# Kernel optimization log

Measured on AMD Instinct MI355X. Metric: run time of the kernel, lower is better.

## Reference

```python
import math
import jax, jax.numpy as jnp
from jax import lax
import numpy as np

NEG_INF = -1e9
LOG_2PI = math.log(2.0 * math.pi)


def compute_logp(z_p, m_p, logs_p):
    # z_p: [B,C,Ty], m_p/logs_p: [B,C,Tx] -> logp: [B,Tx,Ty]
    o_scale = jnp.exp(-2.0 * logs_p)                                  # [B,C,Tx]
    logp1 = jnp.sum(-0.5 * LOG_2PI - logs_p, axis=1)[:, :, None]      # [B,Tx,1]
    logp2 = jnp.einsum('bct,bcs->bts', o_scale, -0.5 * z_p ** 2)      # [B,Tx,Ty]
    logp3 = jnp.einsum('bct,bcs->bts', m_p * o_scale, z_p)            # [B,Tx,Ty]
    logp4 = jnp.sum(-0.5 * m_p ** 2 * o_scale, axis=1)[:, :, None]    # [B,Tx,1]
    return logp1 + logp2 + logp3 + logp4


def maximum_path(logp, mask):
    # Monotonic alignment search (Glow-TTS/VITS Viterbi DP).
    # logp, mask: [B,Tx,Ty]. Returns hard alignment path [B,Tx,Ty] in {0,1}.
    B, Tx, Ty = logp.shape
    tx = mask[:, :, 0].sum(axis=1).astype(jnp.int32)   # text lengths [B]
    ty = mask[:, 0, :].sum(axis=1).astype(jnp.int32)   # mel lengths  [B]
    xs = jnp.arange(Tx, dtype=jnp.int32)

    # ---- forward DP over mel frames y ----
    def fwd(v, inp):
        y, col = inp                                   # col: logp[:, :, y]  [B,Tx]
        v_stay = jnp.where(xs[None, :] == y, NEG_INF, v)           # can't stay on diagonal
        first = jnp.where(y == 0, 0.0, NEG_INF)                     # x==0 boundary
        v_move = jnp.concatenate([jnp.broadcast_to(first, (B, 1)).astype(v.dtype), v[:, :-1]], axis=1)
        newv = jnp.maximum(v_stay, v_move) + col
        # feasible band: x <= y and enough frames remain to consume all text
        feas = (xs[None, :] <= y) & (xs[None, :] >= tx[:, None] + y - ty[:, None])
        newv = jnp.where(feas, newv, NEG_INF)
        return newv, newv

    cols = jnp.moveaxis(logp, 2, 0)                    # [Ty,B,Tx]
    init = jnp.full((B, Tx), NEG_INF, dtype=logp.dtype)
    _, vals = lax.scan(fwd, init, (jnp.arange(Ty, dtype=jnp.int32), cols))  # [Ty,B,Tx]
    prev = jnp.concatenate([jnp.zeros((1, B, Tx), dtype=vals.dtype), vals[:-1]], axis=0)

    # ---- backtrack from (tx-1, ty-1) down to y=0 ----
    def bwd(idx, inp):
        y, pv = inp                                    # pv: value column at y-1  [B,Tx]
        active = y < ty                                # [B] bool
        path_col = (active[:, None] & (xs[None, :] == idx[:, None])).astype(logp.dtype)
        v_stay = jnp.take_along_axis(pv, idx[:, None], axis=1)[:, 0]
        v_move = jnp.take_along_axis(pv, jnp.maximum(idx - 1, 0)[:, None], axis=1)[:, 0]
        dec = (idx != 0) & ((idx == y) | (v_stay < v_move))
        idx = jnp.where(active & dec, idx - 1, idx)
        return idx, path_col

    _, path = lax.scan(bwd, tx - 1, (jnp.arange(Ty, dtype=jnp.int32), prev), reverse=True)
    return jnp.transpose(path, (1, 2, 0))              # [B,Tx,Ty]


def setup_inputs() -> dict:
    key = jax.random.key(0)
    ks = jax.random.split(key, 5)
    B, C, Tx, Ty = 16, 192, 384, 1536
    z_p = jax.random.normal(ks[0], (B, C, Ty), dtype=jnp.float32)
    m_p = jax.random.normal(ks[1], (B, C, Tx), dtype=jnp.float32)
    logs_p = 0.5 * jax.random.normal(ks[2], (B, C, Tx), dtype=jnp.float32)
    x_len = jax.random.randint(ks[3], (B,), Tx // 2, Tx + 1)
    y_len = jax.random.randint(ks[4], (B,), Ty // 2, Ty + 1)  # Ty//2 > Tx -> path always feasible
    x_mask = (jnp.arange(Tx)[None, :] < x_len[:, None]).astype(jnp.float32)[:, None, :]
    y_mask = (jnp.arange(Ty)[None, :] < y_len[:, None]).astype(jnp.float32)[:, None, :]
    return {"z_p": z_p, "m_p": m_p, "logs_p": logs_p, "x_mask": x_mask, "y_mask": y_mask}


def reference(z_p, m_p, logs_p, x_mask, y_mask):
    # forward_mas_without_dp: log-likelihood einsum + monotonic alignment search
    attn_mask = x_mask[:, 0, :, None] * y_mask[:, 0, None, :]   # [B,Tx,Ty]
    logp = compute_logp(z_p, m_p, logs_p)
    attn = maximum_path(logp, attn_mask)
    return attn[:, None]                                         # [B,1,Tx,Ty]
```

## Files before the change

### kernel.cpp

```cpp
#include <hip/hip_runtime.h>
#include <hip/hip_bf16.h>
#include <math.h>

#define NEG_INF (-1e9f)
#define B_   16
#define C_   192
#define TX   384
#define TY   1536
#define NWP  49
#define ROW_BYTES 1536

#define BM 64
#define BN 64
#define BK 16

typedef float f32x2 __attribute__((ext_vector_type(2)));
typedef float f32x4 __attribute__((ext_vector_type(4)));

__global__ __launch_bounds__(64) void k_len(const float* __restrict__ xm,
                                            const float* __restrict__ ym,
                                            int* __restrict__ lens) {
    const int b = blockIdx.x, l = threadIdx.x;
    int tx = 0, ty = 0;
#pragma unroll
    for (int i = 0; i < TX / 64; ++i)
        tx += __popcll(__ballot(xm[b * TX + i * 64 + l] > 0.5f));
#pragma unroll
    for (int i = 0; i < TY / 64; ++i)
        ty += __popcll(__ballot(ym[b * TY + i * 64 + l] > 0.5f));
    if (l == 0) { lens[2 * b] = tx; lens[2 * b + 1] = ty; }
}

__global__ __launch_bounds__(128) void k_rowconst(const float* __restrict__ m_p,
                                                  const float* __restrict__ logs_p,
                                                  float* __restrict__ r) {
    const int b = blockIdx.y;
    const int t = blockIdx.x * 128 + threadIdx.x;
    const float* mp = m_p + b * C_ * TX + t;
    const float* lp = logs_p + b * C_ * TX + t;
    const float c0 = -0.9189385332046727f;
    float s = 0.0f;
    for (int c = 0; c < C_; ++c) {
        float ls = lp[c * TX];
        float m  = mp[c * TX];
        float os = expf(-2.0f * ls);
        s += (c0 - ls) - 0.5f * m * m * os;
    }
    r[b * TX + t] = s;
}

__global__ __launch_bounds__(256) void k_logp(const float* __restrict__ z_p,
                                              const float* __restrict__ m_p,
                                              const float* __restrict__ logs_p,
                                              const float* __restrict__ r,
                                              const int* __restrict__ lens,
                                              float* __restrict__ outT) {
    const int b   = blockIdx.z;
    const int sm0 = blockIdx.y * BM;
    const int ty_len = lens[2 * b + 1];
    if (sm0 >= ((ty_len + 31) & ~31)) return;

    __shared__ float Zs1[BK][BM];
    __shared__ float Zs2[BK][BM];
    __shared__ float Ms1[BK][BN];
    __shared__ float Ms2[BK][BN];

    const int tn0 = blockIdx.x * BN;
    const int tid = threadIdx.x;
    const int lrow = tid >> 4;
    const int lcol = (tid & 15) << 2;
    const int tx_ = tid & 15;
    const int ty_ = tid >> 4;

    const float* mb = m_p + b * C_ * TX;
    const float* lb = logs_p + b * C_ * TX;
    const float* zb = z_p + b * C_ * TY;

    float acc[4][4] = {};

    for (int kk = 0; kk < C_; kk += BK) {
        float4 m4 = *(const float4*)(mb + (kk + lrow) * TX + tn0 + lcol);
        float4 l4 = *(const float4*)(lb + (kk + lrow) * TX + tn0 + lcol);
        float4 z4 = *(const float4*)(zb + (kk + lrow) * TY + sm0 + lcol);

        const float mm[4] = {m4.x, m4.y, m4.z, m4.w};
        const float ll[4] = {l4.x, l4.y, l4.z, l4.w};
        const float zz[4] = {z4.x, z4.y, z4.z, z4.w};
        float osv[4], a2v[4], u1v[4], u2v[4];
#pragma unroll
        for (int i = 0; i < 4; ++i) {
            float os = expf(-2.0f * ll[i]);
            osv[i] = os;
            a2v[i] = mm[i] * os;
            u1v[i] = -0.5f * zz[i] * zz[i];
            u2v[i] = zz[i];
        }

        __syncthreads();
#pragma unroll
        for (int i = 0; i < 4; ++i) {
            Ms1[lrow][lcol + i] = osv[i];
            Ms2[lrow][lcol + i] = a2v[i];
            Zs1[lrow][lcol + i] = u1v[i];
            Zs2[lrow][lcol + i] = u2v[i];
        }
        __syncthreads();

#pragma unroll
        for (int k = 0; k < BK; ++k) {
            float4 z1 = *(const float4*)&Zs1[k][ty_ * 4];
            float4 z2 = *(const float4*)&Zs2[k][ty_ * 4];
            float4 m1 = *(const float4*)&Ms1[k][tx_ * 4];
            float4 m2 = *(const float4*)&Ms2[k][tx_ * 4];
            const float u1a[4] = {z1.x, z1.y, z1.z, z1.w};
            const float u2a[4] = {z2.x, z2.y, z2.z, z2.w};
            const float a1a[4] = {m1.x, m1.y, m1.z, m1.w};
            const float a2a[4] = {m2.x, m2.y, m2.z, m2.w};
#pragma unroll
            for (int i = 0; i < 4; ++i)
#pragma unroll
                for (int j = 0; j < 4; ++j)
                    acc[i][j] = fmaf(a1a[j], u1a[i], fmaf(a2a[j], u2a[i], acc[i][j]));
        }
    }

    float4 r4 = *(const float4*)(r + b * TX + tn0 + tx_ * 4);
    const float rr[4] = {r4.x, r4.y, r4.z, r4.w};
#pragma unroll
    for (int i = 0; i < 4; ++i) {
        const int srow = sm0 + ty_ * 4 + i;
        float4 o;
        o.x = acc[i][0] + rr[0];
        o.y = acc[i][1] + rr[1];
        o.z = acc[i][2] + rr[2];
        o.w = acc[i][3] + rr[3];
        *(float4*)(outT + ((size_t)(b * TY + srow)) * TX + tn0 + tx_ * 4) = o;
    }
}

__global__ __launch_bounds__(64) void k_dp(const float* __restrict__ logpT,
                                           const int* __restrict__ lens,
                                           int* __restrict__ idx_out) {
    extern __shared__ unsigned decw[];

    const int b = blockIdx.x;
    const int l = threadIdx.x;

    const int tx = lens[2 * b];
    const int ty = lens[2 * b + 1];
    const int yend = (ty + 31) & ~31;
    const int NBLK = yend >> 5;

    const char* pl = (const char*)(logpT + (size_t)b * TY * TX) + 24 * l;

    f32x4 Ra[16];
    f32x2 Rb[16];

#define ISSUE_ROW(u, row)                                                        \
    do {                                                                         \
        const char* _p = pl + (size_t)(row) * ROW_BYTES;                         \
        asm volatile("global_load_dwordx4 %0, %1, off"           : "=v"(Ra[u]) : "v"(_p)); \
        asm volatile("global_load_dwordx2 %0, %1, off offset:16" : "=v"(Rb[u]) : "v"(_p)); \
    } while (0)

#pragma unroll
    for (int u = 0; u < 16; ++u) ISSUE_ROW(u, u);

    float v[6];
    unsigned w[6];
#pragma unroll
    for (int k = 0; k < 6; ++k) { v[k] = NEG_INF; w[k] = 0u; }

    float lane0vm = 0.0f;
    const bool is_l0 = (l == 0);

    int nextrow = 16;
    for (int blk = 0; blk < NBLK; ++blk) {
#pragma unroll
        for (int j = 0; j < 32; ++j) {
            const int u = j & 15;
            asm volatile("s_waitcnt vmcnt(30)" : "+v"(Ra[u]), "+v"(Rb[u]));
            float c0 = Ra[u].x, c1 = Ra[u].y, c2 = Ra[u].z;
            float c3 = Ra[u].w, c4 = Rb[u].x, c5 = Rb[u].y;

            const int v5i = __float_as_int(v[5]);
            const int s15 = __builtin_amdgcn_readlane(v5i, 15);
            const int s31 = __builtin_amdgcn_readlane(v5i, 31);
            const int s47 = __builtin_amdgcn_readlane(v5i, 47);
            int vpi = __builtin_amdgcn_update_dpp(0, v5i, 0x111, 0xF, 0xF, false);
            asm("v_writelane_b32 %0, %1, 16" : "+v"(vpi) : "s"(s15));
            asm("v_writelane_b32 %0, %1, 32" : "+v"(vpi) : "s"(s31));
            asm("v_writelane_b32 %0, %1, 48" : "+v"(vpi) : "s"(s47));
            const float vp5 = __int_as_float(vpi);
            const float vm0 = is_l0 ? lane0vm : vp5;

            w[5] = w[5] + w[5] + (v[5] < v[4]);  float n5 = fmaxf(v[5], v[4]) + c5;
            w[4] = w[4] + w[4] + (v[4] < v[3]);  float n4 = fmaxf(v[4], v[3]) + c4;
            w[3] = w[3] + w[3] + (v[3] < v[2]);  float n3 = fmaxf(v[3], v[2]) + c3;
            w[2] = w[2] + w[2] + (v[2] < v[1]);  float n2 = fmaxf(v[2], v[1]) + c2;
            w[1] = w[1] + w[1] + (v[1] < v[0]);  float n1 = fmaxf(v[1], v[0]) + c1;
            w[0] = w[0] + w[0] + (v[0] < vm0);   float n0 = fmaxf(v[0], vm0) + c0;
            v[5] = n5; v[4] = n4; v[3] = n3; v[2] = n2; v[1] = n1; v[0] = n0;

            if (j == 0 && blk == 0) lane0vm = NEG_INF;

            {
                int nr = nextrow < TY ? nextrow : (TY - 1);
                ISSUE_ROW(u, nr);
                ++nextrow;
            }
        }
        const int x0 = 6 * l;
#pragma unroll
        for (int k = 0; k < 6; ++k) { decw[(x0 + k) * NWP + blk] = w[k]; w[k] = 0u; }
    }

    __syncthreads();

    for (int y = ty + l; y < TY; y += 64) idx_out[b * TY + y] = -1;

    if (l == 0) {
        int idx = tx - 1;
        int* io = idx_out + b * TY;
        int blk = (ty - 1) >> 5;
        auto W = [&](int i, int bb) -> unsigned {
            return (i >= 0) ? decw[i * NWP + bb] : 0u;
        };
        unsigned w0 = W(idx, blk), w1 = W(idx - 1, blk),
                 w2 = W(idx - 2, blk), w3 = W(idx - 3, blk);
        for (int y = ty - 1; y >= 0; --y) {
            const int nb = y >> 5;
            if (nb != blk) {
                blk = nb;
                w0 = W(idx, blk); w1 = W(idx - 1, blk);
                w2 = W(idx - 2, blk); w3 = W(idx - 3, blk);
            }
            io[y] = idx;
            if ((w0 >> (31 - (y & 31))) & 1u) {
                --idx;
                w0 = w1; w1 = w2; w2 = w3; w3 = W(idx - 3, blk);
            }
        }
    }
#undef ISSUE_ROW
}

__global__ __launch_bounds__(384) void k_path(const int* __restrict__ idx_arr,
                                              float* __restrict__ out) {
    const int b = blockIdx.y;
    const int x = blockIdx.x;
    const int t = threadIdx.x;
    const int y0 = t * 4;
    int4 iv = *(const int4*)(idx_arr + b * TY + y0);
    float4 o;
    o.x = (iv.x == x) ? 1.0f : 0.0f;
    o.y = (iv.y == x) ? 1.0f : 0.0f;
    o.z = (iv.z == x) ? 1.0f : 0.0f;
    o.w = (iv.w == x) ? 1.0f : 0.0f;
    *(float4*)(out + ((size_t)(b * TX + x)) * TY + y0) = o;
}

extern "C" void kernel_launch(void* const* d_in, const int* in_sizes, int n_in,
                              void* d_out, int out_size, void* d_ws, size_t ws_size,
                              hipStream_t stream) {
    const float* z_p    = (const float*)d_in[0];
    const float* m_p    = (const float*)d_in[1];
    const float* logs_p = (const float*)d_in[2];
    const float* x_mask = (const float*)d_in[3];
    const float* y_mask = (const float*)d_in[4];
    float* out = (float*)d_out;

    float* r       = (float*)d_ws;
    int*   idx_arr = (int*)((char*)d_ws + B_ * TX * 4);
    int*   lens    = (int*)((char*)d_ws + B_ * TX * 4 + B_ * TY * 4);

    static const size_t dp_smem = (size_t)TX * NWP * 4;
    (void)hipFuncSetAttribute((const void*)k_dp,
                              hipFuncAttributeMaxDynamicSharedMemorySize,
                              (int)dp_smem);

    k_len<<<B_, 64, 0, stream>>>(x_mask, y_mask, lens);
    k_rowconst<<<dim3(TX / 128, B_), 128, 0, stream>>>(m_p, logs_p, r);
    k_logp<<<dim3(TX / BN, TY / BM, B_), 256, 0, stream>>>(z_p, m_p, logs_p, r, lens, out);
    k_dp<<<B_, 64, dp_smem, stream>>>(out, lens, idx_arr);
    k_path<<<dim3(TX, B_), TX, 0, stream>>>(idx_arr, out);
}
```

Measured before the change: 367.4 us.

## Warp-specialize DP kernel with producer waves streaming logp rows into LDS ring

The DP kernel grows from a single wave to four. Three producer waves use global_load_lds to stream pairs of logp rows into a 48-row LDS ring buffer, and the consumer wave runs the serial Viterbi recurrence from ds_read results. LDS flags handle the handshake and the consumer waits on them by spin-polling. The aim is to hide global memory latency on the sequential scan, which a single wave's register prefetch of 16 rows covered only partly. The cost is LDS-latency reads, spin-wait overhead, and more shared memory per block.

Result: slower. 420.4 us (+14.4%).

```diff
diff --git a/kernel.cpp b/kernel.cpp
--- a/kernel.cpp
+++ b/kernel.cpp
@@ -9,13 +9,24 @@
 #define TY   1536
 #define NWP  49
 #define ROW_BYTES 1536
+#define RING_ROWS 48
+#define RING_PAIRS 24
+#define RING_BYTES (RING_ROWS * ROW_BYTES)
+#define DECW_BYTES (TX * NWP * 4)
 
 #define BM 64
 #define BN 64
 #define BK 16
 
 typedef float f32x2 __attribute__((ext_vector_type(2)));
-typedef float f32x4 __attribute__((ext_vector_type(4)));
+
+typedef __attribute__((address_space(3))) char* lds_ptr_t;
+typedef __attribute__((address_space(1))) char* glb_ptr_t;
+
+__device__ __forceinline__ void glds16(const char* g, lds_ptr_t l) {
+    __builtin_amdgcn_global_load_lds((__attribute__((address_space(1))) void*)(glb_ptr_t)g,
+                                     (__attribute__((address_space(3))) void*)l, 16, 0, 0);
+}
 
 __global__ __launch_bounds__(64) void k_len(const float* __restrict__ xm,
                                             const float* __restrict__ ym,
@@ -138,51 +149,37 @@
     }
 }
 
-__global__ __launch_bounds__(64) void k_dp(const float* __restrict__ logpT,
-                                           const int* __restrict__ lens,
-                                           int* __restrict__ idx_out) {
-    extern __shared__ unsigned decw[];
-
-    const int b = blockIdx.x;
-    const int l = threadIdx.x;
+__global__ __launch_bounds__(256) void k_dp(const float* __restrict__ logpT,
+                                            const int* __restrict__ lens,
+                                            int* __restrict__ idx_out) {
+    extern __shared__ char smem[];
+    unsigned* decw = (unsigned*)(smem + RING_BYTES);
+    volatile int* flags = (volatile int*)(smem + RING_BYTES + DECW_BYTES);
+
+    const int b   = blockIdx.x;
+    const int tid = threadIdx.x;
+    const int wid = tid >> 6;
+    const int l   = tid & 63;
 
     const int tx = lens[2 * b];
     const int ty = lens[2 * b + 1];
     const int yend = (ty + 31) & ~31;
     const int NBLK = yend >> 5;
 
-    const char* pl = (const char*)(logpT + (size_t)b * TY * TX) + 24 * l;
-
-    f32x4 Ra[16];
-    f32x2 Rb[16];
-
-#define ISSUE_ROW(u, row)                                                        \
-    do {                                                                         \
-        const char* _p = pl + (size_t)(row) * ROW_BYTES;                         \
-        asm volatile("global_load_dwordx4 %0, %1, off"           : "=v"(Ra[u]) : "v"(_p)); \
-        asm volatile("global_load_dwordx2 %0, %1, off offset:16" : "=v"(Rb[u]) : "v"(_p)); \
-    } while (0)
-
-#pragma unroll
-    for (int u = 0; u < 16; ++u) ISSUE_ROW(u, u);
-
-    float v[6];
-    unsigned w[6];
-#pragma unroll
-    for (int k = 0; k < 6; ++k) { v[k] = NEG_INF; w[k] = 0u; }
-
-    float lane0vm = 0.0f;
-    const bool is_l0 = (l == 0);
-
-    int nextrow = 16;
-    for (int blk = 0; blk < NBLK; ++blk) {
-#pragma unroll
-        for (int j = 0; j < 32; ++j) {
-            const int u = j & 15;
-            asm volatile("s_waitcnt vmcnt(30)" : "+v"(Ra[u]), "+v"(Rb[u]));
-            float c0 = Ra[u].x, c1 = Ra[u].y, c2 = Ra[u].z;
-            float c3 = Ra[u].w, c4 = Rb[u].x, c5 = Rb[u].y;
-
+    const char* gb = (const char*)(logpT + (size_t)b * TY * TX);
+
+    if (tid == 0) { flags[0] = -1; flags[1] = -1; flags[2] = -1; flags[3] = 0; }
+    __syncthreads();
+
+    if (wid == 0) {
+        float v[6];
+        unsigned w[6];
+#pragma unroll
+        for (int k = 0; k < 6; ++k) { v[k] = NEG_INF; w[k] = 0u; }
+        float lane0vm = 0.0f;
+        const bool is_l0 = (l == 0);
+
+        auto step = [&](float c0, float c1, float c2, float c3, float c4, float c5, int y) {
             const int v5i = __float_as_int(v[5]);
             const int s15 = __builtin_amdgcn_readlane(v5i, 15);
             const int s31 = __builtin_amdgcn_readlane(v5i, 31);
@@ -193,7 +190,6 @@
             asm("v_writelane_b32 %0, %1, 48" : "+v"(vpi) : "s"(s47));
             const float vp5 = __int_as_float(vpi);
             const float vm0 = is_l0 ? lane0vm : vp5;
-
             w[5] = w[5] + w[5] + (v[5] < v[4]);  float n5 = fmaxf(v[5], v[4]) + c5;
             w[4] = w[4] + w[4] + (v[4] < v[3]);  float n4 = fmaxf(v[4], v[3]) + c4;
             w[3] = w[3] + w[3] + (v[3] < v[2]);  float n3 = fmaxf(v[3], v[2]) + c3;
@@ -201,48 +197,121 @@
             w[1] = w[1] + w[1] + (v[1] < v[0]);  float n1 = fmaxf(v[1], v[0]) + c1;
             w[0] = w[0] + w[0] + (v[0] < vm0);   float n0 = fmaxf(v[0], vm0) + c0;
             v[5] = n5; v[4] = n4; v[3] = n3; v[2] = n2; v[1] = n1; v[0] = n0;
-
-            if (j == 0 && blk == 0) lane0vm = NEG_INF;
-
-            {
-                int nr = nextrow < TY ? nextrow : (TY - 1);
-                ISSUE_ROW(u, nr);
-                ++nextrow;
+            if (y == 0) lane0vm = NEG_INF;
+        };
+
+        f32x2 Da[4], Db[4], Dc[4];
+        int addr = 24 * l;
+        int filled = 0;
+
+        auto waitfill = [&](int need) {
+            if (filled >= need) return;
+            int m;
+            do {
+                int f0 = flags[0], f1 = flags[1], f2 = flags[2];
+                m = f0 < f1 ? f0 : f1; if (f2 < m) m = f2;
+                filled = 2 * (m + 1);
+            } while (filled < need);
+        };
+
+#define ISSUE_RD(s) do {                                                          \
+        asm volatile("ds_read_b64 %0, %3\n\t"                                     \
+                     "ds_read_b64 %1, %3 offset:8\n\t"                            \
+                     "ds_read_b64 %2, %3 offset:16"                               \
+                     : "=v"(Da[s]), "=v"(Db[s]), "=v"(Dc[s]) : "v"(addr));        \
+        addr += ROW_BYTES; if (addr >= RING_BYTES) addr -= RING_BYTES;            \
+    } while (0)
+
+#define CONS(s, n, yy) do {                                                       \
+        asm volatile("s_waitcnt lgkmcnt(" #n ")"                                  \
+                     : "+v"(Da[s]), "+v"(Db[s]), "+v"(Dc[s]));                    \
+        step(Da[s].x, Da[s].y, Db[s].x, Db[s].y, Dc[s].x, Dc[s].y, (yy));         \
+    } while (0)
+
+        waitfill(4);
+        ISSUE_RD(0); ISSUE_RD(1); ISSUE_RD(2); ISSUE_RD(3);
+
+        for (int blk = 0; blk < NBLK; ++blk) {
+            for (int g = 0; g < 4; ++g) {
+                const int base = blk * 32 + g * 8;
+                const bool tail = (base + 8 >= yend);
+                waitfill(tail ? yend : base + 12);
+                if (!tail) {
+                    CONS(0, 9, base + 0); ISSUE_RD(0);
+                    CONS(1, 9, base + 1); ISSUE_RD(1);
+                    CONS(2, 9, base + 2); ISSUE_RD(2);
+                    CONS(3, 9, base + 3); ISSUE_RD(3);
+                    CONS(0, 9, base + 4); ISSUE_RD(0);
+                    CONS(1, 9, base + 5); ISSUE_RD(1);
+                    CONS(2, 9, base + 6); ISSUE_RD(2);
+                    CONS(3, 9, base + 7); ISSUE_RD(3);
+                } else {
+                    CONS(0, 9, base + 0); ISSUE_RD(0);
+                    CONS(1, 9, base + 1); ISSUE_RD(1);
+                    CONS(2, 9, base + 2); ISSUE_RD(2);
+                    CONS(3, 9, base + 3); ISSUE_RD(3);
+                    CONS(0, 9, base + 4);
+                    CONS(1, 6, base + 5);
+                    CONS(2, 3, base + 6);
+                    CONS(3, 0, base + 7);
+                }
+                if (l == 0) flags[3] = base + 8;
             }
-        }
-        const int x0 = 6 * l;
-#pragma unroll
-        for (int k = 0; k < 6; ++k) { decw[(x0 + k) * NWP + blk] = w[k]; w[k] = 0u; }
+            const int x0 = 6 * l;
+#pragma unroll
+            for (int k = 0; k < 6; ++k) { decw[(x0 + k) * NWP + blk] = w[k]; w[k] = 0u; }
+        }
+#undef ISSUE_RD
+#undef CONS
+    } else {
+        const int p = wid - 1;
+        const int npairs = yend >> 1;
+        lds_ptr_t ring = (lds_ptr_t)smem;
+        for (int q = p; q < npairs; q += 3) {
+            if (q >= RING_PAIRS && ((((q - p) / 3) & 1) == 0)) {
+                while (flags[3] < 2 * q - 40) { }
+            }
+            const char* src = gb + (size_t)q * 3072 + 16 * l;
+            lds_ptr_t dst = ring + (q % RING_PAIRS) * 3072;
+            glds16(src,        dst);
+            glds16(src + 1024, dst + 1024);
+            glds16(src + 2048, dst + 2048);
+            asm volatile("s_waitcnt vmcnt(9)" ::: "memory");
+            if (l == 0) flags[p] = q - 3;
+        }
+        asm volatile("s_waitcnt vmcnt(0)" ::: "memory");
+        if (l == 0) flags[p] = 1 << 29;
     }
 
     __syncthreads();
 
-    for (int y = ty + l; y < TY; y += 64) idx_out[b * TY + y] = -1;
-
-    if (l == 0) {
-        int idx = tx - 1;
-        int* io = idx_out + b * TY;
-        int blk = (ty - 1) >> 5;
-        auto W = [&](int i, int bb) -> unsigned {
-            return (i >= 0) ? decw[i * NWP + bb] : 0u;
-        };
-        unsigned w0 = W(idx, blk), w1 = W(idx - 1, blk),
-                 w2 = W(idx - 2, blk), w3 = W(idx - 3, blk);
-        for (int y = ty - 1; y >= 0; --y) {
-            const int nb = y >> 5;
-            if (nb != blk) {
-                blk = nb;
-                w0 = W(idx, blk); w1 = W(idx - 1, blk);
-                w2 = W(idx - 2, blk); w3 = W(idx - 3, blk);
+    if (wid == 0) {
+        for (int y = ty + l; y < TY; y += 64) idx_out[b * TY + y] = -1;
+
+        if (l == 0) {
+            int idx = tx - 1;
+            int* io = idx_out + b * TY;
+            int blk = (ty - 1) >> 5;
+            auto W = [&](int i, int bb) -> unsigned {
+                return (i >= 0) ? decw[i * NWP + bb] : 0u;
+            };
+            unsigned w0 = W(idx, blk), w1 = W(idx - 1, blk),
+                     w2 = W(idx - 2, blk), w3 = W(idx - 3, blk);
+            for (int y = ty - 1; y >= 0; --y) {
+                const int nb = y >> 5;
+                if (nb != blk) {
+                    blk = nb;
+                    w0 = W(idx, blk); w1 = W(idx - 1, blk);
+                    w2 = W(idx - 2, blk); w3 = W(idx - 3, blk);
+                }
+                io[y] = idx;
+                if ((w0 >> (31 - (y & 31))) & 1u) {
+                    --idx;
+                    w0 = w1; w1 = w2; w2 = w3; w3 = W(idx - 3, blk);
+                }
             }
-            io[y] = idx;
-            if ((w0 >> (31 - (y & 31))) & 1u) {
-                --idx;
-                w0 = w1; w1 = w2; w2 = w3; w3 = W(idx - 3, blk);
-            }
-        }
-    }
-#undef ISSUE_ROW
+        }
+    }
 }
 
 __global__ __launch_bounds__(384) void k_path(const int* __restrict__ idx_arr,
@@ -274,7 +343,7 @@
     int*   idx_arr = (int*)((char*)d_ws + B_ * TX * 4);
     int*   lens    = (int*)((char*)d_ws + B_ * TX * 4 + B_ * TY * 4);
 
-    static const size_t dp_smem = (size_t)TX * NWP * 4;
+    static const size_t dp_smem = RING_BYTES + DECW_BYTES + 64;
     (void)hipFuncSetAttribute((const void*)k_dp,
                               hipFuncAttributeMaxDynamicSharedMemorySize,
                               (int)dp_smem);
@@ -282,6 +351,6 @@
     k_len<<<B_, 64, 0, stream>>>(x_mask, y_mask, lens);
     k_rowconst<<<dim3(TX / 128, B_), 128, 0, stream>>>(m_p, logs_p, r);
     k_logp<<<dim3(TX / BN, TY / BM, B_), 256, 0, stream>>>(z_p, m_p, logs_p, r, lens, out);
-    k_dp<<<B_, 64, dp_smem, stream>>>(out, lens, idx_arr);
+    k_dp<<<B_, 256, dp_smem, stream>>>(out, lens, idx_arr);
     k_path<<<dim3(TX, B_), TX, 0, stream>>>(idx_arr, out);
 }
```
